# Performance work log

Hardware: AMD Instinct MI355X
Metric: run time of the kernel (lower is better)

## Reference

```python
import jax, jax.numpy as jnp
import numpy as np

WS = 8      # window_size
NH = 3      # num_heads
SHIFT = True
LN_EPS = 1e-5


def _ln(x, w, b):
    m = jnp.mean(x, axis=-1, keepdims=True)
    v = jnp.mean(jnp.square(x - m), axis=-1, keepdims=True)
    return (x - m) * jax.lax.rsqrt(v + LN_EPS) * w + b


def _window_partition(x):
    B, H, W, C = x.shape
    x = x.reshape(B, H // WS, WS, W // WS, WS, C)
    return x.transpose(0, 1, 3, 2, 4, 5).reshape(-1, WS * WS, C)


def _window_reverse(win, B, H, W):
    C = win.shape[-1]
    x = win.reshape(B, H // WS, W // WS, WS, WS, C)
    return x.transpose(0, 1, 3, 2, 4, 5).reshape(B, H, W, C)


def setup_inputs() -> dict:
    key = jax.random.key(0)
    ks = jax.random.split(key, 6)
    C = 96
    x = jax.random.normal(ks[0], (4, 224, 224, C), dtype=jnp.float32)
    return {
        "x": x,
        "ln1_w": jnp.ones((C,), jnp.float32),
        "ln1_b": jnp.zeros((C,), jnp.float32),
        "in_proj_w": jax.random.normal(ks[1], (3 * C, C), jnp.float32) * 0.02,
        "in_proj_b": jnp.zeros((3 * C,), jnp.float32),
        "out_proj_w": jax.random.normal(ks[2], (C, C), jnp.float32) * 0.02,
        "out_proj_b": jnp.zeros((C,), jnp.float32),
        "ln2_w": jnp.ones((C,), jnp.float32),
        "ln2_b": jnp.zeros((C,), jnp.float32),
        "mlp_w1": jax.random.normal(ks[3], (4 * C, C), jnp.float32) * 0.02,
        "mlp_b1": jnp.zeros((4 * C,), jnp.float32),
        "mlp_w2": jax.random.normal(ks[4], (C, 4 * C), jnp.float32) * 0.02,
        "mlp_b2": jnp.zeros((C,), jnp.float32),
    }


def reference(x, ln1_w, ln1_b, in_proj_w, in_proj_b, out_proj_w, out_proj_b,
              ln2_w, ln2_b, mlp_w1, mlp_b1, mlp_w2, mlp_b2):
    B, H, W, C = x.shape
    hd = C // NH
    s = WS // 2
    if SHIFT:
        x = jnp.roll(x, shift=(-s, -s), axis=(1, 2))
    xw = _window_partition(x)                      # [nw, WS*WS, C]
    h = _ln(xw, ln1_w, ln1_b)
    qkv = h @ in_proj_w.T + in_proj_b              # [nw, L, 3C]
    q, k, v = jnp.split(qkv, 3, axis=-1)
    nw, L = q.shape[0], q.shape[1]
    q = q.reshape(nw, L, NH, hd).transpose(0, 2, 1, 3)
    k = k.reshape(nw, L, NH, hd).transpose(0, 2, 1, 3)
    v = v.reshape(nw, L, NH, hd).transpose(0, 2, 1, 3)
    scores = jnp.einsum('whqd,whkd->whqk', q, k) * (1.0 / np.sqrt(hd))
    attn = jax.nn.softmax(scores, axis=-1)
    o = jnp.einsum('whqk,whkd->whqd', attn, v).transpose(0, 2, 1, 3).reshape(nw, L, C)
    o = o @ out_proj_w.T + out_proj_b
    x = _window_reverse(o, B, H, W)                # attention REPLACES x (no residual, per source)
    if SHIFT:
        x = jnp.roll(x, shift=(s, s), axis=(1, 2))
    h2 = _ln(x, ln2_w, ln2_b)
    mlp = jax.nn.gelu(h2 @ mlp_w1.T + mlp_b1, approximate=False) @ mlp_w2.T + mlp_b2
    return x + mlp
```

## Files before the change

kernel.cpp:

```cpp
#include <hip/hip_runtime.h>
#include <math.h>

static constexpr int Hn   = 224;
static constexpr int Wn   = 224;
static constexpr int Cn   = 96;
static constexpr int Sft  = 4;
static constexpr int NWH  = 28;
static constexpr int NWPB = 784;
static constexpr int NW   = 3136;

typedef __attribute__((ext_vector_type(8))) short bf16x8;
typedef __attribute__((ext_vector_type(4))) float f32x4;
typedef __attribute__((ext_vector_type(4))) short s16x4;

__device__ inline short f2bf(float f) {
    __bf16 h = (__bf16)f;
    return __builtin_bit_cast(short, h);
}

__device__ inline float gelu_f(float a) {
    float u  = a * 0.70710678118654752f;
    float au = fabsf(u);
    float t  = __builtin_amdgcn_rcpf(fmaf(0.3275911f, au, 1.f));
    float e  = __expf(-u * u);
    float p  = t * fmaf(t, fmaf(t, fmaf(t, fmaf(t, 1.061405429f,
                        -1.453152027f), 1.421413741f), -0.284496736f),
                        0.254829592f);
    float er = fmaf(-p, e, 1.f);
    er = (u < 0.f) ? -er : er;
    return 0.5f * a * (1.f + er);
}

__global__ void prep_bf16(const float* __restrict__ wqkv, const float* __restrict__ wo,
                          const float* __restrict__ w1,   const float* __restrict__ w2,
                          short* __restrict__ ws) {
    int idx = blockIdx.x * 256 + threadIdx.x;
    if (idx < 27648)        ws[idx] = f2bf(wqkv[idx]);
    else if (idx < 36864)   ws[idx] = f2bf(wo[idx - 27648]);
    else if (idx < 73728)   ws[idx] = f2bf(w1[idx - 36864]);
    else if (idx < 110592)  ws[idx] = f2bf(w2[idx - 73728]);
}

static constexpr int LDH  = 104;
static constexpr int LDQK = 200;
static constexpr int LDVT = 72;
static constexpr int LDP  = 200;
static constexpr int LDXF = 100;
static constexpr int LDST = 100;
static constexpr int LDAQ = 104;

__global__ __launch_bounds__(256, 3) void attn_mlp(
    const float* __restrict__ x,
    const float* __restrict__ ln1w, const float* __restrict__ ln1b,
    const short* __restrict__ wqb,  const float* __restrict__ bqkv,
    const short* __restrict__ wob,  const float* __restrict__ bo,
    const float* __restrict__ ln2w, const float* __restrict__ ln2b,
    const short* __restrict__ w1b,  const float* __restrict__ b1,
    const short* __restrict__ w2b,  const float* __restrict__ b2,
    float* __restrict__ out)
{
    __shared__ __align__(16) char  U[64 * 400];
    __shared__ __align__(16) short h2b[64 * LDH];
    __shared__ __align__(16) short vtact[96 * LDVT];
    __shared__ int   tbase[64];

    const int blk = blockIdx.x;
    const int b   = blk / NWPB;
    const int rem = blk - b * NWPB;
    const int wh  = rem / NWH;
    const int ww  = rem - wh * NWH;
    const int tid  = threadIdx.x;
    const int lane = tid & 63;
    const int wv   = __builtin_amdgcn_readfirstlane(tid >> 6);
    const int lr   = lane & 15;
    const int lk   = lane >> 4;
    const int wr   = wv >> 1;
    const int wc   = wv & 1;

    if (tid < 64) {
        int i = tid >> 3, j = tid & 7;
        int hs = wh * 8 + i + Sft; if (hs >= Hn) hs -= Hn;
        int ws2 = ww * 8 + j + Sft; if (ws2 >= Wn) ws2 -= Wn;
        tbase[tid] = ((b * Hn + hs) * Wn + ws2) * Cn;
    }
    __syncthreads();

    float* xf = (float*)U;
    for (int i = tid; i < 64 * 24; i += 256) {
        int row = i / 24, c4 = i - row * 24;
        float4 v = ((const float4*)(x + tbase[row]))[c4];
        *(float4*)&xf[row * LDXF + c4 * 4] = v;
    }
    __syncthreads();

    {
        const int l = tid >> 2, p = tid & 3;
        float s0 = 0.f, s1 = 0.f;
        #pragma unroll
        for (int c0 = 0; c0 < 24; ++c0) {
            float v = xf[l * LDXF + p * 24 + c0];
            s0 += v; s1 += v * v;
        }
        s0 += __shfl_xor(s0, 1); s1 += __shfl_xor(s1, 1);
        s0 += __shfl_xor(s0, 2); s1 += __shfl_xor(s1, 2);
        float mean = s0 * (1.f / 96.f);
        float var  = fmaxf(s1 * (1.f / 96.f) - mean * mean, 0.f);
        float rstd = rsqrtf(var + 1e-5f);
        #pragma unroll
        for (int c0 = 0; c0 < 24; ++c0) {
            int c = p * 24 + c0;
            float v = xf[l * LDXF + c];
            h2b[l * LDH + c] = f2bf((v - mean) * rstd * ln1w[c] + ln1b[c]);
        }
    }
    __syncthreads();

    short* qk = (short*)U;
    short* vt = vtact;
    {
        bf16x8 aq[2][3];
        #pragma unroll
        for (int rt = 0; rt < 2; ++rt)
            #pragma unroll
            for (int ks = 0; ks < 3; ++ks)
                aq[rt][ks] = *(const bf16x8*)&h2b[(wr * 32 + rt * 16 + lr) * LDH + ks * 32 + lk * 8];

        #pragma unroll 3
        for (int ct9 = 0; ct9 < 9; ++ct9) {
            const int ct = wc * 9 + ct9;
            const short* bp = wqb + (ct * 16 + lr) * 96 + lk * 8;
            bf16x8 b0 = *(const bf16x8*)(bp);
            bf16x8 b1 = *(const bf16x8*)(bp + 32);
            bf16x8 b2v = *(const bf16x8*)(bp + 64);
            if (ct < 12) {
                const float4 b4 = *(const float4*)&bqkv[ct * 16 + lk * 4];
                #pragma unroll
                for (int rt = 0; rt < 2; ++rt) {
                    f32x4 acc = (f32x4){0.f, 0.f, 0.f, 0.f};
                    acc = __builtin_amdgcn_mfma_f32_16x16x32_bf16(b0, aq[rt][0], acc, 0, 0, 0);
                    acc = __builtin_amdgcn_mfma_f32_16x16x32_bf16(b1, aq[rt][1], acc, 0, 0, 0);
                    acc = __builtin_amdgcn_mfma_f32_16x16x32_bf16(b2v, aq[rt][2], acc, 0, 0, 0);
                    const int tok = wr * 32 + rt * 16 + lr;
                    s16x4 pk;
                    pk[0] = f2bf(acc[0] + b4.x); pk[1] = f2bf(acc[1] + b4.y);
                    pk[2] = f2bf(acc[2] + b4.z); pk[3] = f2bf(acc[3] + b4.w);
                    *(s16x4*)&qk[tok * LDQK + ct * 16 + lk * 4] = pk;
                }
            } else {
                const float bs = bqkv[ct * 16 + lr];
                #pragma unroll
                for (int rt = 0; rt < 2; ++rt) {
                    f32x4 acc = (f32x4){0.f, 0.f, 0.f, 0.f};
                    acc = __builtin_amdgcn_mfma_f32_16x16x32_bf16(aq[rt][0], b0, acc, 0, 0, 0);
                    acc = __builtin_amdgcn_mfma_f32_16x16x32_bf16(aq[rt][1], b1, acc, 0, 0, 0);
                    acc = __builtin_amdgcn_mfma_f32_16x16x32_bf16(aq[rt][2], b2v, acc, 0, 0, 0);
                    const int rb = wr * 32 + rt * 16;
                    s16x4 pk;
                    #pragma unroll
                    for (int r = 0; r < 4; ++r) pk[r] = f2bf(acc[r] + bs);
                    *(s16x4*)&vt[(ct * 16 + lr - 192) * LDVT + rb + lk * 4] = pk;
                }
            }
        }
    }
    __syncthreads();

    short* pb = (short*)U;
    {
        f32x4 accs[3][4];
        #pragma unroll
        for (int h = 0; h < 3; ++h) {
            bf16x8 aqf = *(const bf16x8*)&qk[(wv * 16 + lr) * LDQK + h * 32 + lk * 8];
            #pragma unroll
            for (int ct = 0; ct < 4; ++ct) {
                bf16x8 bk = *(const bf16x8*)&qk[(ct * 16 + lr) * LDQK + 96 + h * 32 + lk * 8];
                f32x4 z = (f32x4){0.f, 0.f, 0.f, 0.f};
                accs[h][ct] = __builtin_amdgcn_mfma_f32_16x16x32_bf16(aqf, bk, z, 0, 0, 0);
            }
        }
        __syncthreads();

        const float scale = 0.17677669529663687f;
        float inv[3][4];
        #pragma unroll
        for (int h = 0; h < 3; ++h) {
            #pragma unroll
            for (int r = 0; r < 4; ++r) {
                float m = fmaxf(fmaxf(accs[h][0][r], accs[h][1][r]),
                                fmaxf(accs[h][2][r], accs[h][3][r]));
                m = fmaxf(m, __shfl_xor(m, 1));
                m = fmaxf(m, __shfl_xor(m, 2));
                m = fmaxf(m, __shfl_xor(m, 4));
                m = fmaxf(m, __shfl_xor(m, 8));
                float s = 0.f;
                #pragma unroll
                for (int ct = 0; ct < 4; ++ct) {
                    float p = __expf((accs[h][ct][r] - m) * scale);
                    accs[h][ct][r] = p; s += p;
                }
                s += __shfl_xor(s, 1); s += __shfl_xor(s, 2);
                s += __shfl_xor(s, 4); s += __shfl_xor(s, 8);
                inv[h][r] = 1.f / s;
            }
        }
        #pragma unroll
        for (int h = 0; h < 3; ++h)
            #pragma unroll
            for (int ct = 0; ct < 4; ++ct)
                #pragma unroll
                for (int r = 0; r < 4; ++r)
                    pb[(wv * 16 + lk * 4 + r) * LDP + h * 64 + ct * 16 + lr] =
                        f2bf(accs[h][ct][r]);

        f32x4 acco[3][2];
        #pragma unroll
        for (int h = 0; h < 3; ++h)
            #pragma unroll
            for (int ct = 0; ct < 2; ++ct) acco[h][ct] = (f32x4){0.f, 0.f, 0.f, 0.f};
        #pragma unroll
        for (int h = 0; h < 3; ++h) {
            #pragma unroll
            for (int ks = 0; ks < 2; ++ks) {
                bf16x8 ap = *(const bf16x8*)&pb[(wv * 16 + lr) * LDP + h * 64 + ks * 32 + lk * 8];
                #pragma unroll
                for (int ct = 0; ct < 2; ++ct) {
                    bf16x8 bv = *(const bf16x8*)&vt[(h * 32 + ct * 16 + lr) * LDVT + ks * 32 + lk * 8];
                    acco[h][ct] = __builtin_amdgcn_mfma_f32_16x16x32_bf16(ap, bv, acco[h][ct], 0, 0, 0);
                }
            }
        }
        #pragma unroll
        for (int h = 0; h < 3; ++h)
            #pragma unroll
            for (int ct = 0; ct < 2; ++ct)
                #pragma unroll
                for (int r = 0; r < 4; ++r)
                    h2b[(wv * 16 + lk * 4 + r) * LDH + h * 32 + ct * 16 + lr] =
                        f2bf(acco[h][ct][r] * inv[h][r]);
    }

    float* st = (float*)U;
    {
        bf16x8 o0 = *(const bf16x8*)&h2b[(wv * 16 + lr) * LDH +  0 + lk * 8];
        bf16x8 o1 = *(const bf16x8*)&h2b[(wv * 16 + lr) * LDH + 32 + lk * 8];
        bf16x8 o2 = *(const bf16x8*)&h2b[(wv * 16 + lr) * LDH + 64 + lk * 8];
        #pragma unroll
        for (int ct = 0; ct < 6; ++ct) {
            const short* bp = wob + (ct * 16 + lr) * 96 + lk * 8;
            bf16x8 b0 = *(const bf16x8*)(bp);
            bf16x8 b1 = *(const bf16x8*)(bp + 32);
            bf16x8 b2v = *(const bf16x8*)(bp + 64);
            f32x4 acc = (f32x4){0.f, 0.f, 0.f, 0.f};
            acc = __builtin_amdgcn_mfma_f32_16x16x32_bf16(b0, o0, acc, 0, 0, 0);
            acc = __builtin_amdgcn_mfma_f32_16x16x32_bf16(b1, o1, acc, 0, 0, 0);
            acc = __builtin_amdgcn_mfma_f32_16x16x32_bf16(b2v, o2, acc, 0, 0, 0);
            const float4 b4 = *(const float4*)&bo[ct * 16 + lk * 4];
            float4 v;
            v.x = acc[0] + b4.x; v.y = acc[1] + b4.y;
            v.z = acc[2] + b4.z; v.w = acc[3] + b4.w;
            *(float4*)&st[(wv * 16 + lr) * LDST + ct * 16 + lk * 4] = v;
        }
    }

    {
        const int l = tid >> 2, p = tid & 3;
        float s0 = 0.f, s1 = 0.f;
        #pragma unroll
        for (int c0 = 0; c0 < 24; ++c0) {
            float v = st[l * LDST + p * 24 + c0];
            s0 += v; s1 += v * v;
        }
        s0 += __shfl_xor(s0, 1); s1 += __shfl_xor(s1, 1);
        s0 += __shfl_xor(s0, 2); s1 += __shfl_xor(s1, 2);
        float mean = s0 * (1.f / 96.f);
        float var  = fmaxf(s1 * (1.f / 96.f) - mean * mean, 0.f);
        float rstd = rsqrtf(var + 1e-5f);
        #pragma unroll
        for (int c0 = 0; c0 < 24; ++c0) {
            int c = p * 24 + c0;
            float v = st[l * LDST + c];
            h2b[l * LDH + c] = f2bf((v - mean) * rstd * ln2w[c] + ln2b[c]);
        }
    }
    __syncthreads();

    short* actQ0 = vtact;
    short* actQ1 = h2b;
    bf16x8 a1[4][3];
    #pragma unroll
    for (int rt = 0; rt < 4; ++rt)
        #pragma unroll
        for (int ks = 0; ks < 3; ++ks)
            a1[rt][ks] = *(const bf16x8*)&h2b[(rt * 16 + lr) * LDH + ks * 32 + lk * 8];

    f32x4 acc2[2][3];
    #pragma unroll
    for (int rt = 0; rt < 2; ++rt)
        #pragma unroll
        for (int ct = 0; ct < 3; ++ct) acc2[rt][ct] = (f32x4){0.f, 0.f, 0.f, 0.f};

    for (int half = 0; half < 2; ++half) {
        const int oc0w = half * 192 + wv * 48;
        f32x4 acc1[4][3];
        #pragma unroll
        for (int rt = 0; rt < 4; ++rt)
            #pragma unroll
            for (int ct = 0; ct < 3; ++ct) acc1[rt][ct] = (f32x4){0.f, 0.f, 0.f, 0.f};

        #pragma unroll
        for (int ct = 0; ct < 3; ++ct) {
            const short* bp = w1b + (oc0w + ct * 16 + lr) * 96 + lk * 8;
            bf16x8 bg0 = *(const bf16x8*)(bp);
            bf16x8 bg1 = *(const bf16x8*)(bp + 32);
            bf16x8 bg2 = *(const bf16x8*)(bp + 64);
            #pragma unroll
            for (int rt = 0; rt < 4; ++rt) {
                acc1[rt][ct] = __builtin_amdgcn_mfma_f32_16x16x32_bf16(bg0, a1[rt][0], acc1[rt][ct], 0, 0, 0);
                acc1[rt][ct] = __builtin_amdgcn_mfma_f32_16x16x32_bf16(bg1, a1[rt][1], acc1[rt][ct], 0, 0, 0);
                acc1[rt][ct] = __builtin_amdgcn_mfma_f32_16x16x32_bf16(bg2, a1[rt][2], acc1[rt][ct], 0, 0, 0);
            }
        }

        for (int sub = 0; sub < 2; ++sub) {
            short* actQ = (sub == 0) ? actQ0 : actQ1;
            if (wr == sub) {
                #pragma unroll
                for (int ct = 0; ct < 3; ++ct) {
                    const float4 b14 = *(const float4*)&b1[oc0w + ct * 16 + lk * 4];
                    const int lcolb = wc * 48 + ct * 16 + lk * 4;
                    #pragma unroll
                    for (int rt = 0; rt < 4; ++rt) {
                        s16x4 pk;
                        pk[0] = f2bf(gelu_f(acc1[rt][ct][0] + b14.x));
                        pk[1] = f2bf(gelu_f(acc1[rt][ct][1] + b14.y));
                        pk[2] = f2bf(gelu_f(acc1[rt][ct][2] + b14.z));
                        pk[3] = f2bf(gelu_f(acc1[rt][ct][3] + b14.w));
                        *(s16x4*)&actQ[(rt * 16 + lr) * LDAQ + lcolb] = pk;
                    }
                }
            }
            __syncthreads();

            #pragma unroll
            for (int ks = 0; ks < 3; ++ks) {
                bf16x8 a2[2];
                #pragma unroll
                for (int rt = 0; rt < 2; ++rt)
                    a2[rt] = *(const bf16x8*)&actQ[(wr * 32 + rt * 16 + lr) * LDAQ + ks * 32 + lk * 8];
                #pragma unroll
                for (int ct = 0; ct < 3; ++ct) {
                    bf16x8 bw = *(const bf16x8*)(w2b + (wc * 48 + ct * 16 + lr) * 384
                                                  + half * 192 + sub * 96 + ks * 32 + lk * 8);
                    #pragma unroll
                    for (int rt = 0; rt < 2; ++rt)
                        acc2[rt][ct] = __builtin_amdgcn_mfma_f32_16x16x32_bf16(bw, a2[rt], acc2[rt][ct], 0, 0, 0);
                }
            }
        }
    }

    #pragma unroll
    for (int ct = 0; ct < 3; ++ct) {
        const int colb = wc * 48 + ct * 16 + lk * 4;
        const float4 b24 = *(const float4*)&b2[colb];
        #pragma unroll
        for (int rt = 0; rt < 2; ++rt) {
            const int row = wr * 32 + rt * 16 + lr;
            float4 v = *(const float4*)&st[row * LDST + colb];
            v.x += acc2[rt][ct][0] + b24.x;
            v.y += acc2[rt][ct][1] + b24.y;
            v.z += acc2[rt][ct][2] + b24.z;
            v.w += acc2[rt][ct][3] + b24.w;
            *(float4*)&st[row * LDST + colb] = v;
        }
    }
    __syncthreads();

    for (int i = tid; i < 64 * 96; i += 256) {
        int l = i / 96, c = i - l * 96;
        out[tbase[l] + c] = st[l * LDST + c];
    }
}

extern "C" void kernel_launch(void* const* d_in, const int* in_sizes, int n_in,
                              void* d_out, int out_size, void* d_ws, size_t ws_size,
                              hipStream_t stream) {
    const float* x    = (const float*)d_in[0];
    const float* ln1w = (const float*)d_in[1];
    const float* ln1b = (const float*)d_in[2];
    const float* wqkv = (const float*)d_in[3];
    const float* bqkv = (const float*)d_in[4];
    const float* wo   = (const float*)d_in[5];
    const float* bo   = (const float*)d_in[6];
    const float* ln2w = (const float*)d_in[7];
    const float* ln2b = (const float*)d_in[8];
    const float* w1   = (const float*)d_in[9];
    const float* b1   = (const float*)d_in[10];
    const float* w2   = (const float*)d_in[11];
    const float* b2   = (const float*)d_in[12];
    float* out = (float*)d_out;

    short* ws  = (short*)d_ws;
    short* wqb = ws;
    short* wob = ws + 27648;
    short* w1b = ws + 36864;
    short* w2b = ws + 73728;

    prep_bf16<<<432, 256, 0, stream>>>(wqkv, wo, w1, w2, ws);
    attn_mlp<<<NW, 256, 0, stream>>>(x, ln1w, ln1b, wqb, bqkv, wob, bo,
                                     ln2w, ln2b, w1b, b1, w2b, b2, out);
}
```

Measured before the change: 187.6 us.

## Make attention-MLP kernel persistent and prefetch next window's input into registers

The kernel now launches a fixed grid of 768 blocks that loop over the 3136 windows. Each block prefetches the next window's x tile into registers while the current window is computed. Input loads and output stores become per-thread float4 row accesses, which removes the shared tbase table and one barrier. The aim is to hide global load latency and cut block launch overhead. In exchange, register pressure goes up and the 3136 windows do not divide evenly across blocks, leaving a tail imbalance.

```diff
diff --git a/kernel.cpp b/kernel.cpp
--- a/kernel.cpp
+++ b/kernel.cpp
@@ -8,6 +8,7 @@
 static constexpr int NWH  = 28;
 static constexpr int NWPB = 784;
 static constexpr int NW   = 3136;
+static constexpr int GRID = 768;
 
 typedef __attribute__((ext_vector_type(8))) short bf16x8;
 typedef __attribute__((ext_vector_type(4))) float f32x4;
@@ -62,13 +63,7 @@
     __shared__ __align__(16) char  U[64 * 400];
     __shared__ __align__(16) short h2b[64 * LDH];
     __shared__ __align__(16) short vtact[96 * LDVT];
-    __shared__ int   tbase[64];
-
-    const int blk = blockIdx.x;
-    const int b   = blk / NWPB;
-    const int rem = blk - b * NWPB;
-    const int wh  = rem / NWH;
-    const int ww  = rem - wh * NWH;
+
     const int tid  = threadIdx.x;
     const int lane = tid & 63;
     const int wv   = __builtin_amdgcn_readfirstlane(tid >> 6);
@@ -76,309 +71,339 @@
     const int lk   = lane >> 4;
     const int wr   = wv >> 1;
     const int wc   = wv & 1;
-
-    if (tid < 64) {
-        int i = tid >> 3, j = tid & 7;
-        int hs = wh * 8 + i + Sft; if (hs >= Hn) hs -= Hn;
-        int ws2 = ww * 8 + j + Sft; if (ws2 >= Wn) ws2 -= Wn;
-        tbase[tid] = ((b * Hn + hs) * Wn + ws2) * Cn;
+    const int lt   = tid >> 2;
+    const int lp   = tid & 3;
+    const int ti   = lt >> 3, tj = lt & 7;
+
+    int w = blockIdx.x;
+    int tb;
+    float4 vpre[6];
+    {
+        int b = w / NWPB, rem = w - b * NWPB;
+        int wh = rem / NWH, ww = rem - wh * NWH;
+        int hs  = wh * 8 + ti + Sft; if (hs  >= Hn) hs  -= Hn;
+        int ws2 = ww * 8 + tj + Sft; if (ws2 >= Wn) ws2 -= Wn;
+        tb = ((b * Hn + hs) * Wn + ws2) * Cn;
+        const float4* xp = (const float4*)(x + tb + lp * 24);
+        #pragma unroll
+        for (int jj = 0; jj < 6; ++jj) vpre[jj] = xp[jj];
     }
-    __syncthreads();
-
-    float* xf = (float*)U;
-    for (int i = tid; i < 64 * 24; i += 256) {
-        int row = i / 24, c4 = i - row * 24;
-        float4 v = ((const float4*)(x + tbase[row]))[c4];
-        *(float4*)&xf[row * LDXF + c4 * 4] = v;
-    }
-    __syncthreads();
-
-    {
-        const int l = tid >> 2, p = tid & 3;
-        float s0 = 0.f, s1 = 0.f;
+
+    for (; w < NW; w += GRID) {
+        float* xf = (float*)U;
         #pragma unroll
-        for (int c0 = 0; c0 < 24; ++c0) {
-            float v = xf[l * LDXF + p * 24 + c0];
-            s0 += v; s1 += v * v;
-        }
-        s0 += __shfl_xor(s0, 1); s1 += __shfl_xor(s1, 1);
-        s0 += __shfl_xor(s0, 2); s1 += __shfl_xor(s1, 2);
-        float mean = s0 * (1.f / 96.f);
-        float var  = fmaxf(s1 * (1.f / 96.f) - mean * mean, 0.f);
-        float rstd = rsqrtf(var + 1e-5f);
+        for (int jj = 0; jj < 6; ++jj)
+            *(float4*)&xf[lt * LDXF + lp * 24 + jj * 4] = vpre[jj];
+        __syncthreads();
+
+        {
+            const int l = lt, p = lp;
+            float s0 = 0.f, s1 = 0.f;
+            #pragma unroll
+            for (int c0 = 0; c0 < 24; ++c0) {
+                float v = xf[l * LDXF + p * 24 + c0];
+                s0 += v; s1 += v * v;
+            }
+            s0 += __shfl_xor(s0, 1); s1 += __shfl_xor(s1, 1);
+            s0 += __shfl_xor(s0, 2); s1 += __shfl_xor(s1, 2);
+            float mean = s0 * (1.f / 96.f);
+            float var  = fmaxf(s1 * (1.f / 96.f) - mean * mean, 0.f);
+            float rstd = rsqrtf(var + 1e-5f);
+            #pragma unroll
+            for (int c0 = 0; c0 < 24; ++c0) {
+                int c = p * 24 + c0;
+                float v = xf[l * LDXF + c];
+                h2b[l * LDH + c] = f2bf((v - mean) * rstd * ln1w[c] + ln1b[c]);
+            }
+        }
+
+        int tbn = 0;
+        {
+            const int wn = w + GRID;
+            if (wn < NW) {
+                int b = wn / NWPB, rem = wn - b * NWPB;
+                int wh = rem / NWH, ww = rem - wh * NWH;
+                int hs  = wh * 8 + ti + Sft; if (hs  >= Hn) hs  -= Hn;
+                int ws2 = ww * 8 + tj + Sft; if (ws2 >= Wn) ws2 -= Wn;
+                tbn = ((b * Hn + hs) * Wn + ws2) * Cn;
+                const float4* xp = (const float4*)(x + tbn + lp * 24);
+                #pragma unroll
+                for (int jj = 0; jj < 6; ++jj) vpre[jj] = xp[jj];
+            }
+        }
+        __syncthreads();
+
+        short* qk = (short*)U;
+        short* vt = vtact;
+        {
+            bf16x8 aq[2][3];
+            #pragma unroll
+            for (int rt = 0; rt < 2; ++rt)
+                #pragma unroll
+                for (int ks = 0; ks < 3; ++ks)
+                    aq[rt][ks] = *(const bf16x8*)&h2b[(wr * 32 + rt * 16 + lr) * LDH + ks * 32 + lk * 8];
+
+            #pragma unroll 3
+            for (int ct9 = 0; ct9 < 9; ++ct9) {
+                const int ct = wc * 9 + ct9;
+                const short* bp = wqb + (ct * 16 + lr) * 96 + lk * 8;
+                bf16x8 b0 = *(const bf16x8*)(bp);
+                bf16x8 b1 = *(const bf16x8*)(bp + 32);
+                bf16x8 b2v = *(const bf16x8*)(bp + 64);
+                if (ct < 12) {
+                    const float4 b4 = *(const float4*)&bqkv[ct * 16 + lk * 4];
+                    #pragma unroll
+                    for (int rt = 0; rt < 2; ++rt) {
+                        f32x4 acc = (f32x4){0.f, 0.f, 0.f, 0.f};
+                        acc = __builtin_amdgcn_mfma_f32_16x16x32_bf16(b0, aq[rt][0], acc, 0, 0, 0);
+                        acc = __builtin_amdgcn_mfma_f32_16x16x32_bf16(b1, aq[rt][1], acc, 0, 0, 0);
+                        acc = __builtin_amdgcn_mfma_f32_16x16x32_bf16(b2v, aq[rt][2], acc, 0, 0, 0);
+                        const int tok = wr * 32 + rt * 16 + lr;
+                        s16x4 pk;
+                        pk[0] = f2bf(acc[0] + b4.x); pk[1] = f2bf(acc[1] + b4.y);
+                        pk[2] = f2bf(acc[2] + b4.z); pk[3] = f2bf(acc[3] + b4.w);
+                        *(s16x4*)&qk[tok * LDQK + ct * 16 + lk * 4] = pk;
+                    }
+                } else {
+                    const float bs = bqkv[ct * 16 + lr];
+                    #pragma unroll
+                    for (int rt = 0; rt < 2; ++rt) {
+                        f32x4 acc = (f32x4){0.f, 0.f, 0.f, 0.f};
+                        acc = __builtin_amdgcn_mfma_f32_16x16x32_bf16(aq[rt][0], b0, acc, 0, 0, 0);
+                        acc = __builtin_amdgcn_mfma_f32_16x16x32_bf16(aq[rt][1], b1, acc, 0, 0, 0);
+                        acc = __builtin_amdgcn_mfma_f32_16x16x32_bf16(aq[rt][2], b2v, acc, 0, 0, 0);
+                        const int rb = wr * 32 + rt * 16;
+                        s16x4 pk;
+                        #pragma unroll
+                        for (int r = 0; r < 4; ++r) pk[r] = f2bf(acc[r] + bs);
+                        *(s16x4*)&vt[(ct * 16 + lr - 192) * LDVT + rb + lk * 4] = pk;
+                    }
+                }
+            }
+        }
+        __syncthreads();
+
+        short* pb = (short*)U;
+        {
+            f32x4 accs[3][4];
+            #pragma unroll
+            for (int h = 0; h < 3; ++h) {
+                bf16x8 aqf = *(const bf16x8*)&qk[(wv * 16 + lr) * LDQK + h * 32 + lk * 8];
+                #pragma unroll
+                for (int ct = 0; ct < 4; ++ct) {
+                    bf16x8 bk = *(const bf16x8*)&qk[(ct * 16 + lr) * LDQK + 96 + h * 32 + lk * 8];
+                    f32x4 z = (f32x4){0.f, 0.f, 0.f, 0.f};
+                    accs[h][ct] = __builtin_amdgcn_mfma_f32_16x16x32_bf16(aqf, bk, z, 0, 0, 0);
+                }
+            }
+            __syncthreads();
+
+            const float scale = 0.17677669529663687f;
+            float inv[3][4];
+            #pragma unroll
+            for (int h = 0; h < 3; ++h) {
+                #pragma unroll
+                for (int r = 0; r < 4; ++r) {
+                    float m = fmaxf(fmaxf(accs[h][0][r], accs[h][1][r]),
+                                    fmaxf(accs[h][2][r], accs[h][3][r]));
+                    m = fmaxf(m, __shfl_xor(m, 1));
+                    m = fmaxf(m, __shfl_xor(m, 2));
+                    m = fmaxf(m, __shfl_xor(m, 4));
+                    m = fmaxf(m, __shfl_xor(m, 8));
+                    float s = 0.f;
+                    #pragma unroll
+                    for (int ct = 0; ct < 4; ++ct) {
+                        float p = __expf((accs[h][ct][r] - m) * scale);
+                        accs[h][ct][r] = p; s += p;
+                    }
+                    s += __shfl_xor(s, 1); s += __shfl_xor(s, 2);
+                    s += __shfl_xor(s, 4); s += __shfl_xor(s, 8);
+                    inv[h][r] = 1.f / s;
+                }
+            }
+            #pragma unroll
+            for (int h = 0; h < 3; ++h)
+                #pragma unroll
+                for (int ct = 0; ct < 4; ++ct)
+                    #pragma unroll
+                    for (int r = 0; r < 4; ++r)
+                        pb[(wv * 16 + lk * 4 + r) * LDP + h * 64 + ct * 16 + lr] =
+                            f2bf(accs[h][ct][r]);
+
+            f32x4 acco[3][2];
+            #pragma unroll
+            for (int h = 0; h < 3; ++h)
+                #pragma unroll
+                for (int ct = 0; ct < 2; ++ct) acco[h][ct] = (f32x4){0.f, 0.f, 0.f, 0.f};
+            #pragma unroll
+            for (int h = 0; h < 3; ++h) {
+                #pragma unroll
+                for (int ks = 0; ks < 2; ++ks) {
+                    bf16x8 ap = *(const bf16x8*)&pb[(wv * 16 + lr) * LDP + h * 64 + ks * 32 + lk * 8];
+                    #pragma unroll
+                    for (int ct = 0; ct < 2; ++ct) {
+                        bf16x8 bv = *(const bf16x8*)&vt[(h * 32 + ct * 16 + lr) * LDVT + ks * 32 + lk * 8];
+                        acco[h][ct] = __builtin_amdgcn_mfma_f32_16x16x32_bf16(ap, bv, acco[h][ct], 0, 0, 0);
+                    }
+                }
+            }
+            #pragma unroll
+            for (int h = 0; h < 3; ++h)
+                #pragma unroll
+                for (int ct = 0; ct < 2; ++ct)
+                    #pragma unroll
+                    for (int r = 0; r < 4; ++r)
+                        h2b[(wv * 16 + lk * 4 + r) * LDH + h * 32 + ct * 16 + lr] =
+                            f2bf(acco[h][ct][r] * inv[h][r]);
+        }
+
+        float* st = (float*)U;
+        {
+            bf16x8 o0 = *(const bf16x8*)&h2b[(wv * 16 + lr) * LDH +  0 + lk * 8];
+            bf16x8 o1 = *(const bf16x8*)&h2b[(wv * 16 + lr) * LDH + 32 + lk * 8];
+            bf16x8 o2 = *(const bf16x8*)&h2b[(wv * 16 + lr) * LDH + 64 + lk * 8];
+            #pragma unroll
+            for (int ct = 0; ct < 6; ++ct) {
+                const short* bp = wob + (ct * 16 + lr) * 96 + lk * 8;
+                bf16x8 b0 = *(const bf16x8*)(bp);
+                bf16x8 b1 = *(const bf16x8*)(bp + 32);
+                bf16x8 b2v = *(const bf16x8*)(bp + 64);
+                f32x4 acc = (f32x4){0.f, 0.f, 0.f, 0.f};
+                acc = __builtin_amdgcn_mfma_f32_16x16x32_bf16(b0, o0, acc, 0, 0, 0);
+                acc = __builtin_amdgcn_mfma_f32_16x16x32_bf16(b1, o1, acc, 0, 0, 0);
+                acc = __builtin_amdgcn_mfma_f32_16x16x32_bf16(b2v, o2, acc, 0, 0, 0);
+                const float4 b4 = *(const float4*)&bo[ct * 16 + lk * 4];
+                float4 v;
+                v.x = acc[0] + b4.x; v.y = acc[1] + b4.y;
+                v.z = acc[2] + b4.z; v.w = acc[3] + b4.w;
+                *(float4*)&st[(wv * 16 + lr) * LDST + ct * 16 + lk * 4] = v;
+            }
+        }
+
+        {
+            const int l = lt, p = lp;
+            float s0 = 0.f, s1 = 0.f;
+            #pragma unroll
+            for (int c0 = 0; c0 < 24; ++c0) {
+                float v = st[l * LDST + p * 24 + c0];
+                s0 += v; s1 += v * v;
+            }
+            s0 += __shfl_xor(s0, 1); s1 += __shfl_xor(s1, 1);
+            s0 += __shfl_xor(s0, 2); s1 += __shfl_xor(s1, 2);
+            float mean = s0 * (1.f / 96.f);
+            float var  = fmaxf(s1 * (1.f / 96.f) - mean * mean, 0.f);
+            float rstd = rsqrtf(var + 1e-5f);
+            #pragma unroll
+            for (int c0 = 0; c0 < 24; ++c0) {
+                int c = p * 24 + c0;
+                float v = st[l * LDST + c];
+                h2b[l * LDH + c] = f2bf((v - mean) * rstd * ln2w[c] + ln2b[c]);
+            }
+        }
+        __syncthreads();
+
+        short* actQ0 = vtact;
+        short* actQ1 = h2b;
+        bf16x8 a1[4][3];
         #pragma unroll
-        for (int c0 = 0; c0 < 24; ++c0) {
-            int c = p * 24 + c0;
-            float v = xf[l * LDXF + c];
-            h2b[l * LDH + c] = f2bf((v - mean) * rstd * ln1w[c] + ln1b[c]);
-        }
-    }
-    __syncthreads();
-
-    short* qk = (short*)U;
-    short* vt = vtact;
-    {
-        bf16x8 aq[2][3];
+        for (int rt = 0; rt < 4; ++rt)
+            #pragma unroll
+            for (int ks = 0; ks < 3; ++ks)
+                a1[rt][ks] = *(const bf16x8*)&h2b[(rt * 16 + lr) * LDH + ks * 32 + lk * 8];
+
+        f32x4 acc2[2][3];
         #pragma unroll
         for (int rt = 0; rt < 2; ++rt)
             #pragma unroll
-            for (int ks = 0; ks < 3; ++ks)
-                aq[rt][ks] = *(const bf16x8*)&h2b[(wr * 32 + rt * 16 + lr) * LDH + ks * 32 + lk * 8];
-
-        #pragma unroll 3
-        for (int ct9 = 0; ct9 < 9; ++ct9) {
-            const int ct = wc * 9 + ct9;
-            const short* bp = wqb + (ct * 16 + lr) * 96 + lk * 8;
-            bf16x8 b0 = *(const bf16x8*)(bp);
-            bf16x8 b1 = *(const bf16x8*)(bp + 32);
-            bf16x8 b2v = *(const bf16x8*)(bp + 64);
-            if (ct < 12) {
-                const float4 b4 = *(const float4*)&bqkv[ct * 16 + lk * 4];
-                #pragma unroll
-                for (int rt = 0; rt < 2; ++rt) {
-                    f32x4 acc = (f32x4){0.f, 0.f, 0.f, 0.f};
-                    acc = __builtin_amdgcn_mfma_f32_16x16x32_bf16(b0, aq[rt][0], acc, 0, 0, 0);
-                    acc = __builtin_amdgcn_mfma_f32_16x16x32_bf16(b1, aq[rt][1], acc, 0, 0, 0);
-                    acc = __builtin_amdgcn_mfma_f32_16x16x32_bf16(b2v, aq[rt][2], acc, 0, 0, 0);
-                    const int tok = wr * 32 + rt * 16 + lr;
-                    s16x4 pk;
-                    pk[0] = f2bf(acc[0] + b4.x); pk[1] = f2bf(acc[1] + b4.y);
-                    pk[2] = f2bf(acc[2] + b4.z); pk[3] = f2bf(acc[3] + b4.w);
-                    *(s16x4*)&qk[tok * LDQK + ct * 16 + lk * 4] = pk;
-                }
-            } else {
-                const float bs = bqkv[ct * 16 + lr];
-                #pragma unroll
-                for (int rt = 0; rt < 2; ++rt) {
-                    f32x4 acc = (f32x4){0.f, 0.f, 0.f, 0.f};
-                    acc = __builtin_amdgcn_mfma_f32_16x16x32_bf16(aq[rt][0], b0, acc, 0, 0, 0);
-                    acc = __builtin_amdgcn_mfma_f32_16x16x32_bf16(aq[rt][1], b1, acc, 0, 0, 0);
-                    acc = __builtin_amdgcn_mfma_f32_16x16x32_bf16(aq[rt][2], b2v, acc, 0, 0, 0);
-                    const int rb = wr * 32 + rt * 16;
-                    s16x4 pk;
-                    #pragma unroll
-                    for (int r = 0; r < 4; ++r) pk[r] = f2bf(acc[r] + bs);
-                    *(s16x4*)&vt[(ct * 16 + lr - 192) * LDVT + rb + lk * 4] = pk;
-                }
-            }
-        }
-    }
-    __syncthreads();
-
-    short* pb = (short*)U;
-    {
-        f32x4 accs[3][4];
-        #pragma unroll
-        for (int h = 0; h < 3; ++h) {
-            bf16x8 aqf = *(const bf16x8*)&qk[(wv * 16 + lr) * LDQK + h * 32 + lk * 8];
-            #pragma unroll
-            for (int ct = 0; ct < 4; ++ct) {
-                bf16x8 bk = *(const bf16x8*)&qk[(ct * 16 + lr) * LDQK + 96 + h * 32 + lk * 8];
-                f32x4 z = (f32x4){0.f, 0.f, 0.f, 0.f};
-                accs[h][ct] = __builtin_amdgcn_mfma_f32_16x16x32_bf16(aqf, bk, z, 0, 0, 0);
-            }
-        }
-        __syncthreads();
-
-        const float scale = 0.17677669529663687f;
-        float inv[3][4];
-        #pragma unroll
-        for (int h = 0; h < 3; ++h) {
-            #pragma unroll
-            for (int r = 0; r < 4; ++r) {
-                float m = fmaxf(fmaxf(accs[h][0][r], accs[h][1][r]),
-                                fmaxf(accs[h][2][r], accs[h][3][r]));
-                m = fmaxf(m, __shfl_xor(m, 1));
-                m = fmaxf(m, __shfl_xor(m, 2));
-                m = fmaxf(m, __shfl_xor(m, 4));
-                m = fmaxf(m, __shfl_xor(m, 8));
-                float s = 0.f;
-                #pragma unroll
-                for (int ct = 0; ct < 4; ++ct) {
-                    float p = __expf((accs[h][ct][r] - m) * scale);
-                    accs[h][ct][r] = p; s += p;
-                }
-                s += __shfl_xor(s, 1); s += __shfl_xor(s, 2);
-                s += __shfl_xor(s, 4); s += __shfl_xor(s, 8);
-                inv[h][r] = 1.f / s;
-            }
-        }
-        #pragma unroll
-        for (int h = 0; h < 3; ++h)
-            #pragma unroll
-            for (int ct = 0; ct < 4; ++ct)
-                #pragma unroll
-                for (int r = 0; r < 4; ++r)
-                    pb[(wv * 16 + lk * 4 + r) * LDP + h * 64 + ct * 16 + lr] =
-                        f2bf(accs[h][ct][r]);
-
-        f32x4 acco[3][2];
-        #pragma unroll
-        for (int h = 0; h < 3; ++h)
-            #pragma unroll
-            for (int ct = 0; ct < 2; ++ct) acco[h][ct] = (f32x4){0.f, 0.f, 0.f, 0.f};
-        #pragma unroll
-        for (int h = 0; h < 3; ++h) {
-            #pragma unroll
-            for (int ks = 0; ks < 2; ++ks) {
-                bf16x8 ap = *(const bf16x8*)&pb[(wv * 16 + lr) * LDP + h * 64 + ks * 32 + lk * 8];
-                #pragma unroll
-                for (int ct = 0; ct < 2; ++ct) {
-                    bf16x8 bv = *(const bf16x8*)&vt[(h * 32 + ct * 16 + lr) * LDVT + ks * 32 + lk * 8];
-                    acco[h][ct] = __builtin_amdgcn_mfma_f32_16x16x32_bf16(ap, bv, acco[h][ct], 0, 0, 0);
-                }
-            }
-        }
-        #pragma unroll
-        for (int h = 0; h < 3; ++h)
-            #pragma unroll
-            for (int ct = 0; ct < 2; ++ct)
-                #pragma unroll
-                for (int r = 0; r < 4; ++r)
-                    h2b[(wv * 16 + lk * 4 + r) * LDH + h * 32 + ct * 16 + lr] =
-                        f2bf(acco[h][ct][r] * inv[h][r]);
-    }
-
-    float* st = (float*)U;
-    {
-        bf16x8 o0 = *(const bf16x8*)&h2b[(wv * 16 + lr) * LDH +  0 + lk * 8];
-        bf16x8 o1 = *(const bf16x8*)&h2b[(wv * 16 + lr) * LDH + 32 + lk * 8];
-        bf16x8 o2 = *(const bf16x8*)&h2b[(wv * 16 + lr) * LDH + 64 + lk * 8];
-        #pragma unroll
-        for (int ct = 0; ct < 6; ++ct) {
-            const short* bp = wob + (ct * 16 + lr) * 96 + lk * 8;
-            bf16x8 b0 = *(const bf16x8*)(bp);
-            bf16x8 b1 = *(const bf16x8*)(bp + 32);
-            bf16x8 b2v = *(const bf16x8*)(bp + 64);
-            f32x4 acc = (f32x4){0.f, 0.f, 0.f, 0.f};
-            acc = __builtin_amdgcn_mfma_f32_16x16x32_bf16(b0, o0, acc, 0, 0, 0);
-            acc = __builtin_amdgcn_mfma_f32_16x16x32_bf16(b1, o1, acc, 0, 0, 0);
-            acc = __builtin_amdgcn_mfma_f32_16x16x32_bf16(b2v, o2, acc, 0, 0, 0);
-            const float4 b4 = *(const float4*)&bo[ct * 16 + lk * 4];
-            float4 v;
-            v.x = acc[0] + b4.x; v.y = acc[1] + b4.y;
-            v.z = acc[2] + b4.z; v.w = acc[3] + b4.w;
-            *(float4*)&st[(wv * 16 + lr) * LDST + ct * 16 + lk * 4] = v;
-        }
-    }
-
-    {
-        const int l = tid >> 2, p = tid & 3;
-        float s0 = 0.f, s1 = 0.f;
-        #pragma unroll
-        for (int c0 = 0; c0 < 24; ++c0) {
-            float v = st[l * LDST + p * 24 + c0];
-            s0 += v; s1 += v * v;
-        }
-        s0 += __shfl_xor(s0, 1); s1 += __shfl_xor(s1, 1);
-        s0 += __shfl_xor(s0, 2); s1 += __shfl_xor(s1, 2);
-        float mean = s0 * (1.f / 96.f);
-        float var  = fmaxf(s1 * (1.f / 96.f) - mean * mean, 0.f);
-        float rstd = rsqrtf(var + 1e-5f);
-        #pragma unroll
-        for (int c0 = 0; c0 < 24; ++c0) {
-            int c = p * 24 + c0;
-            float v = st[l * LDST + c];
-            h2b[l * LDH + c] = f2bf((v - mean) * rstd * ln2w[c] + ln2b[c]);
-        }
-    }
-    __syncthreads();
-
-    short* actQ0 = vtact;
-    short* actQ1 = h2b;
-    bf16x8 a1[4][3];
-    #pragma unroll
-    for (int rt = 0; rt < 4; ++rt)
-        #pragma unroll
-        for (int ks = 0; ks < 3; ++ks)
-            a1[rt][ks] = *(const bf16x8*)&h2b[(rt * 16 + lr) * LDH + ks * 32 + lk * 8];
-
-    f32x4 acc2[2][3];
-    #pragma unroll
-    for (int rt = 0; rt < 2; ++rt)
-        #pragma unroll
-        for (int ct = 0; ct < 3; ++ct) acc2[rt][ct] = (f32x4){0.f, 0.f, 0.f, 0.f};
-
-    for (int half = 0; half < 2; ++half) {
-        const int oc0w = half * 192 + wv * 48;
-        f32x4 acc1[4][3];
-        #pragma unroll
-        for (int rt = 0; rt < 4; ++rt)
-            #pragma unroll
-            for (int ct = 0; ct < 3; ++ct) acc1[rt][ct] = (f32x4){0.f, 0.f, 0.f, 0.f};
+            for (int ct = 0; ct < 3; ++ct) acc2[rt][ct] = (f32x4){0.f, 0.f, 0.f, 0.f};
+
+        for (int half = 0; half < 2; ++half) {
+            const int oc0w = half * 192 + wv * 48;
+            f32x4 acc1[4][3];
+            #pragma unroll
+            for (int rt = 0; rt < 4; ++rt)
+                #pragma unroll
+                for (int ct = 0; ct < 3; ++ct) acc1[rt][ct] = (f32x4){0.f, 0.f, 0.f, 0.f};
+
+            #pragma unroll
+            for (int ct = 0; ct < 3; ++ct) {
+                const short* bp = w1b + (oc0w + ct * 16 + lr) * 96 + lk * 8;
+                bf16x8 bg0 = *(const bf16x8*)(bp);
+                bf16x8 bg1 = *(const bf16x8*)(bp + 32);
+                bf16x8 bg2 = *(const bf16x8*)(bp + 64);
+                #pragma unroll
+                for (int rt = 0; rt < 4; ++rt) {
+                    acc1[rt][ct] = __builtin_amdgcn_mfma_f32_16x16x32_bf16(bg0, a1[rt][0], acc1[rt][ct], 0, 0, 0);
+                    acc1[rt][ct] = __builtin_amdgcn_mfma_f32_16x16x32_bf16(bg1, a1[rt][1], acc1[rt][ct], 0, 0, 0);
+                    acc1[rt][ct] = __builtin_amdgcn_mfma_f32_16x16x32_bf16(bg2, a1[rt][2], acc1[rt][ct], 0, 0, 0);
+                }
+            }
+
+            for (int sub = 0; sub < 2; ++sub) {
+                short* actQ = (sub == 0) ? actQ0 : actQ1;
+                if (wr == sub) {
+                    #pragma unroll
+                    for (int ct = 0; ct < 3; ++ct) {
+                        const float4 b14 = *(const float4*)&b1[oc0w + ct * 16 + lk * 4];
+                        const int lcolb = wc * 48 + ct * 16 + lk * 4;
+                        #pragma unroll
+                        for (int rt = 0; rt < 4; ++rt) {
+                            s16x4 pk;
+                            pk[0] = f2bf(gelu_f(acc1[rt][ct][0] + b14.x));
+                            pk[1] = f2bf(gelu_f(acc1[rt][ct][1] + b14.y));
+                            pk[2] = f2bf(gelu_f(acc1[rt][ct][2] + b14.z));
+                            pk[3] = f2bf(gelu_f(acc1[rt][ct][3] + b14.w));
+                            *(s16x4*)&actQ[(rt * 16 + lr) * LDAQ + lcolb] = pk;
+                        }
+                    }
+                }
+                __syncthreads();
+
+                #pragma unroll
+                for (int ks = 0; ks < 3; ++ks) {
+                    bf16x8 a2[2];
+                    #pragma unroll
+                    for (int rt = 0; rt < 2; ++rt)
+                        a2[rt] = *(const bf16x8*)&actQ[(wr * 32 + rt * 16 + lr) * LDAQ + ks * 32 + lk * 8];
+                    #pragma unroll
+                    for (int ct = 0; ct < 3; ++ct) {
+                        bf16x8 bw = *(const bf16x8*)(w2b + (wc * 48 + ct * 16 + lr) * 384
+                                                      + half * 192 + sub * 96 + ks * 32 + lk * 8);
+                        #pragma unroll
+                        for (int rt = 0; rt < 2; ++rt)
+                            acc2[rt][ct] = __builtin_amdgcn_mfma_f32_16x16x32_bf16(bw, a2[rt], acc2[rt][ct], 0, 0, 0);
+                    }
+                }
+            }
+        }
 
         #pragma unroll
         for (int ct = 0; ct < 3; ++ct) {
-            const short* bp = w1b + (oc0w + ct * 16 + lr) * 96 + lk * 8;
-            bf16x8 bg0 = *(const bf16x8*)(bp);
-            bf16x8 bg1 = *(const bf16x8*)(bp + 32);
-            bf16x8 bg2 = *(const bf16x8*)(bp + 64);
-            #pragma unroll
-            for (int rt = 0; rt < 4; ++rt) {
-                acc1[rt][ct] = __builtin_amdgcn_mfma_f32_16x16x32_bf16(bg0, a1[rt][0], acc1[rt][ct], 0, 0, 0);
-                acc1[rt][ct] = __builtin_amdgcn_mfma_f32_16x16x32_bf16(bg1, a1[rt][1], acc1[rt][ct], 0, 0, 0);
-                acc1[rt][ct] = __builtin_amdgcn_mfma_f32_16x16x32_bf16(bg2, a1[rt][2], acc1[rt][ct], 0, 0, 0);
-            }
-        }
-
-        for (int sub = 0; sub < 2; ++sub) {
-            short* actQ = (sub == 0) ? actQ0 : actQ1;
-            if (wr == sub) {
-                #pragma unroll
-                for (int ct = 0; ct < 3; ++ct) {
-                    const float4 b14 = *(const float4*)&b1[oc0w + ct * 16 + lk * 4];
-                    const int lcolb = wc * 48 + ct * 16 + lk * 4;
-                    #pragma unroll
-                    for (int rt = 0; rt < 4; ++rt) {
-                        s16x4 pk;
-                        pk[0] = f2bf(gelu_f(acc1[rt][ct][0] + b14.x));
-                        pk[1] = f2bf(gelu_f(acc1[rt][ct][1] + b14.y));
-                        pk[2] = f2bf(gelu_f(acc1[rt][ct][2] + b14.z));
-                        pk[3] = f2bf(gelu_f(acc1[rt][ct][3] + b14.w));
-                        *(s16x4*)&actQ[(rt * 16 + lr) * LDAQ + lcolb] = pk;
-                    }
-                }
-            }
-            __syncthreads();
-
-            #pragma unroll
-            for (int ks = 0; ks < 3; ++ks) {
-                bf16x8 a2[2];
-                #pragma unroll
-                for (int rt = 0; rt < 2; ++rt)
-                    a2[rt] = *(const bf16x8*)&actQ[(wr * 32 + rt * 16 + lr) * LDAQ + ks * 32 + lk * 8];
-                #pragma unroll
-                for (int ct = 0; ct < 3; ++ct) {
-                    bf16x8 bw = *(const bf16x8*)(w2b + (wc * 48 + ct * 16 + lr) * 384
-                                                  + half * 192 + sub * 96 + ks * 32 + lk * 8);
-                    #pragma unroll
-                    for (int rt = 0; rt < 2; ++rt)
-                        acc2[rt][ct] = __builtin_amdgcn_mfma_f32_16x16x32_bf16(bw, a2[rt], acc2[rt][ct], 0, 0, 0);
-                }
-            }
-        }
-    }
-
-    #pragma unroll
-    for (int ct = 0; ct < 3; ++ct) {
-        const int colb = wc * 48 + ct * 16 + lk * 4;
-        const float4 b24 = *(const float4*)&b2[colb];
-        #pragma unroll
-        for (int rt = 0; rt < 2; ++rt) {
-            const int row = wr * 32 + rt * 16 + lr;
-            float4 v = *(const float4*)&st[row * LDST + colb];
-            v.x += acc2[rt][ct][0] + b24.x;
-            v.y += acc2[rt][ct][1] + b24.y;
-            v.z += acc2[rt][ct][2] + b24.z;
-            v.w += acc2[rt][ct][3] + b24.w;
-            *(float4*)&st[row * LDST + colb] = v;
-        }
-    }
-    __syncthreads();
-
-    for (int i = tid; i < 64 * 96; i += 256) {
-        int l = i / 96, c = i - l * 96;
-        out[tbase[l] + c] = st[l * LDST + c];
+            const int colb = wc * 48 + ct * 16 + lk * 4;
+            const float4 b24 = *(const float4*)&b2[colb];
+            #pragma unroll
+            for (int rt = 0; rt < 2; ++rt) {
+                const int row = wr * 32 + rt * 16 + lr;
+                float4 v = *(const float4*)&st[row * LDST + colb];
+                v.x += acc2[rt][ct][0] + b24.x;
+                v.y += acc2[rt][ct][1] + b24.y;
+                v.z += acc2[rt][ct][2] + b24.z;
+                v.w += acc2[rt][ct][3] + b24.w;
+                *(float4*)&st[row * LDST + colb] = v;
+            }
+        }
+        __syncthreads();
+
+        {
+            const float* srow = &st[lt * LDST + lp * 24];
+            float* orow = out + tb + lp * 24;
+            #pragma unroll
+            for (int jj = 0; jj < 6; ++jj)
+                ((float4*)orow)[jj] = ((const float4*)srow)[jj];
+        }
+        __syncthreads();
+
+        tb = tbn;
     }
 }
 
@@ -407,6 +432,6 @@
     short* w2b = ws + 73728;
 
     prep_bf16<<<432, 256, 0, stream>>>(wqkv, wo, w1, w2, ws);
-    attn_mlp<<<NW, 256, 0, stream>>>(x, ln1w, ln1b, wqb, bqkv, wob, bo,
-                                     ln2w, ln2b, w1b, b1, w2b, b2, out);
+    attn_mlp<<<GRID, 256, 0, stream>>>(x, ln1w, ln1b, wqb, bqkv, wob, bo,
+                                       ln2w, ln2b, w1b, b1, w2b, b2, out);
 }
```

Result: slower. 390.0 us (+107.9%).
